# Kernel tuning notes

Measured on AMD Instinct MI355X. Metric: run time of the kernel, lower is better.

Reference implementation:

```python
import jax, jax.numpy as jnp
import numpy as np

B, S, D, M, E, K = 2, 2048, 1024, 1408, 8, 2  # batch, seq, n_embed, n_moe_mlp, n_experts, top_k


def setup_inputs() -> dict:
    key = jax.random.key(0)
    k0, k1, k2, k3, k4 = jax.random.split(key, 5)
    scale = 0.02
    return {
        "x": jax.random.normal(k0, (B, S, D), dtype=jnp.float32),
        "w_gate": jax.random.normal(k1, (D, E), dtype=jnp.float32) * scale,  # gate.weight.T
        "w_g": jax.random.normal(k2, (E, D, M), dtype=jnp.float32) * scale,  # gate_proj.weight.T per expert
        "w_u": jax.random.normal(k3, (E, D, M), dtype=jnp.float32) * scale,  # up_proj.weight.T per expert
        "w_d": jax.random.normal(k4, (E, M, D), dtype=jnp.float32) * scale,  # down_proj.weight.T per expert
    }


def reference(x, w_gate, w_g, w_u, w_d):
    # router
    scores = x @ w_gate                                  # [B,S,E]
    topk_scores, topk_idx = jax.lax.top_k(scores, K)     # [B,S,K]
    topk_probs = jax.nn.softmax(topk_scores, axis=-1)    # softmax over selected experts only
    # scatter top-k probs back to dense [B,S,E] gating (top_k indices are distinct)
    gating = jnp.sum(
        jax.nn.one_hot(topk_idx, E, dtype=topk_probs.dtype) * topk_probs[..., None],
        axis=-2,
    )                                                    # [B,S,E]
    # dense all-expert SwiGLU (faithful to the compute-then-mask original)
    hidden = jax.nn.silu(jnp.einsum("bsd,edm->ebsm", x, w_g)) * jnp.einsum(
        "bsd,edm->ebsm", x, w_u
    )                                                    # [E,B,S,M]
    expert_out = jnp.einsum("ebsm,emd->ebsd", hidden, w_d)  # [E,B,S,D]
    # masked weighted combine
    y = jnp.einsum("bse,ebsd->bsd", gating, expert_out)  # [B,S,D]
    return y
```

## Files before the change

### kernel.cpp

```cpp
#include <hip/hip_runtime.h>
#include <cstdio>

constexpr int T  = 4096;
constexpr int D  = 1024;
constexpr int M  = 1408;
constexpr int E  = 8;

constexpr int TM = 128;
constexpr int TN = 128;
constexpr int BK = 64;
constexpr int RCAP = T * 2 + E * TM;
constexpr int MT_MAX = T / TM;
constexpr int NT_UP = M / TN;
constexpr int NT_DN = D / TN;

constexpr int CSTR = 64;
constexpr int TOKB = 16;
constexpr int RTB  = T / TOKB;
constexpr int TP_PER_W = (M / 32) * (D / 32) * E;
constexpr int PREP_GRID = RTB + 3 * TP_PER_W;

typedef _Float16 half8 __attribute__((ext_vector_type(8)));
typedef _Float16 half4 __attribute__((ext_vector_type(4)));
typedef float    floatx4 __attribute__((ext_vector_type(4)));

constexpr size_t OFF_COUNTS = 0;
constexpr size_t OFF_BASE   = (size_t)E * CSTR * 4;
constexpr size_t OFF_PC     = OFF_BASE + 64;
constexpr size_t OFF_TOTAL  = OFF_PC + 64;
constexpr size_t OFF_T2E    = OFF_TOTAL + 64;
constexpr size_t OFF_T2POS  = OFF_T2E   + (size_t)2 * T * 4;
constexpr size_t OFF_T2P    = OFF_T2POS + (size_t)2 * T * 4;
constexpr size_t OFF_TLIST  = OFF_T2P   + (size_t)2 * T * 4;
constexpr size_t OFF_XG     = OFF_TLIST + (size_t)E * T * 4;
constexpr size_t OFF_HID    = OFF_XG  + (size_t)RCAP * D * 2;
constexpr size_t OFF_WGT    = OFF_HID + (size_t)RCAP * M * 2;
constexpr size_t OFF_WUT    = OFF_WGT + (size_t)E * M * D * 2;
constexpr size_t OFF_WDT    = OFF_WUT + (size_t)E * M * D * 2;
constexpr size_t WS_NEED    = OFF_WDT + (size_t)E * D * M * 2;

__device__ __forceinline__ void gl_lds16(const void* g, void* l) {
  __builtin_amdgcn_global_load_lds(
      (const __attribute__((address_space(1))) unsigned int*)g,
      (__attribute__((address_space(3))) unsigned int*)l, 16, 0, 0);
}

__device__ __forceinline__ void expert_base_pc(const int* __restrict__ counts,
                                               int e, int& base_e, int& pc_e) {
  int b = 0; base_e = 0; pc_e = 0;
  #pragma unroll
  for (int ee = 0; ee < E; ++ee) {
    int c = counts[ee * CSTR];
    int p = (c + TM - 1) / TM * TM;
    if (ee == e) { base_e = b; pc_e = p; }
    b += p;
  }
}

__global__ __launch_bounds__(256) void k_prep(
    const float* __restrict__ x, const float* __restrict__ wgate,
    const float* __restrict__ w_g, const float* __restrict__ w_u,
    const float* __restrict__ w_d,
    _Float16* __restrict__ wgT, _Float16* __restrict__ wuT, _Float16* __restrict__ wdT,
    int* __restrict__ counts, int* __restrict__ tlist,
    int* __restrict__ t2e, int* __restrict__ t2pos, float* __restrict__ t2p) {
  __shared__ float tile[32][33];
  __shared__ int   s_cnt[E];
  __shared__ int   s_base[E];
  __shared__ int   s_e[2 * TOKB];
  __shared__ int   s_pos[2 * TOKB];
  __shared__ float s_p[2 * TOKB];
  int bid = blockIdx.x;

  if (bid < RTB) {
    int wv = threadIdx.x >> 6, lane = threadIdx.x & 63;
    if (threadIdx.x < E) s_cnt[threadIdx.x] = 0;
    __syncthreads();
    for (int j = 0; j < TOKB / 4; ++j) {
      int tl = wv * (TOKB / 4) + j;
      int t  = bid * TOKB + tl;
      const float* xr = x + (size_t)t * D;
      float acc[E] = {0.f,0.f,0.f,0.f,0.f,0.f,0.f,0.f};
      #pragma unroll
      for (int i = 0; i < D / 64; ++i) {
        int d = i * 64 + lane;
        float xv = xr[d];
        const float4* wr2 = (const float4*)(wgate + (size_t)d * E);
        float4 w0 = wr2[0], w1 = wr2[1];
        acc[0] += xv * w0.x; acc[1] += xv * w0.y; acc[2] += xv * w0.z; acc[3] += xv * w0.w;
        acc[4] += xv * w1.x; acc[5] += xv * w1.y; acc[6] += xv * w1.z; acc[7] += xv * w1.w;
      }
      #pragma unroll
      for (int e = 0; e < E; ++e) {
        #pragma unroll
        for (int off = 32; off; off >>= 1) acc[e] += __shfl_xor(acc[e], off, 64);
      }
      if (lane == 0) {
        int i0 = 0; float s0 = acc[0];
        #pragma unroll
        for (int e = 1; e < E; ++e) if (acc[e] > s0) { s0 = acc[e]; i0 = e; }
        int i1 = -1; float s1 = -1e30f;
        #pragma unroll
        for (int e = 0; e < E; ++e) if (e != i0 && acc[e] > s1) { s1 = acc[e]; i1 = e; }
        float p0 = 1.f / (1.f + expf(s1 - s0));
        float p1 = 1.f - p0;
        int q0 = atomicAdd(&s_cnt[i0], 1);
        int q1 = atomicAdd(&s_cnt[i1], 1);
        s_e[2 * tl]     = i0; s_pos[2 * tl]     = q0; s_p[2 * tl]     = p0;
        s_e[2 * tl + 1] = i1; s_pos[2 * tl + 1] = q1; s_p[2 * tl + 1] = p1;
      }
    }
    __syncthreads();
    if (threadIdx.x < E)
      s_base[threadIdx.x] = atomicAdd(&counts[threadIdx.x * CSTR], s_cnt[threadIdx.x]);
    __syncthreads();
    if (threadIdx.x < 2 * TOKB) {
      int sl = threadIdx.x;
      int e = s_e[sl];
      int pos = s_base[e] + s_pos[sl];
      int t = bid * TOKB + (sl >> 1);
      tlist[e * T + pos] = t;
      t2e[2 * t + (sl & 1)]   = e;
      t2pos[2 * t + (sl & 1)] = pos;
      t2p[2 * t + (sl & 1)]   = s_p[sl];
    }
    return;
  }

  int i = bid - RTB;
  int which = i / TP_PER_W;
  int j = i - which * TP_PER_W;
  const float* src; _Float16* dst; int Rr, Cc;
  if (which == 0)      { src = w_g; dst = wgT; Rr = D; Cc = M; }
  else if (which == 1) { src = w_u; dst = wuT; Rr = D; Cc = M; }
  else                 { src = w_d; dst = wdT; Rr = M; Cc = D; }
  int ctn = Cc / 32, rtn = Rr / 32;
  int e   = j / (ctn * rtn);
  int rem = j - e * (ctn * rtn);
  int rt = rem / ctn, ct = rem - rt * ctn;
  int tr  = threadIdx.x >> 3;
  int tc4 = (threadIdx.x & 7) * 4;
  const float* s = src + ((size_t)e * Rr + rt * 32 + tr) * Cc + ct * 32 + tc4;
  float4 v = *(const float4*)s;
  tile[tr][tc4 + 0] = v.x; tile[tr][tc4 + 1] = v.y;
  tile[tr][tc4 + 2] = v.z; tile[tr][tc4 + 3] = v.w;
  __syncthreads();
  union { _Float16 h[4]; ushort4 u; } o;
  #pragma unroll
  for (int q = 0; q < 4; ++q) o.h[q] = (_Float16)tile[tc4 + q][tr];
  *(ushort4*)(dst + ((size_t)e * Cc + ct * 32 + tr) * Rr + rt * 32 + tc4) = o.u;
}

__global__ __launch_bounds__(256) void k_gather(
    const float* __restrict__ x, const int* __restrict__ counts,
    const int* __restrict__ tlist, _Float16* __restrict__ Xg) {
  int r = blockIdx.x;
  int b = 0, e = -1, local = 0, cnt = 0;
  #pragma unroll
  for (int ee = 0; ee < E; ++ee) {
    int c = counts[ee * CSTR];
    int p = (c + TM - 1) / TM * TM;
    if (e < 0 && r < b + p) { e = ee; local = r - b; cnt = c; }
    b += p;
  }
  if (e < 0) return;
  int d = threadIdx.x * 4;
  union { _Float16 h[4]; ushort4 u; } o;
  if (local < cnt) {
    int t = tlist[e * T + local];
    float4 v = *(const float4*)(x + (size_t)t * D + d);
    o.h[0] = (_Float16)v.x; o.h[1] = (_Float16)v.y;
    o.h[2] = (_Float16)v.z; o.h[3] = (_Float16)v.w;
  } else {
    o.h[0] = (_Float16)0.f; o.h[1] = (_Float16)0.f;
    o.h[2] = (_Float16)0.f; o.h[3] = (_Float16)0.f;
  }
  *(ushort4*)(Xg + (size_t)r * D + d) = o.u;
}

__global__ __launch_bounds__(256, 2) void k_upgate(
    const _Float16* __restrict__ Xg, const _Float16* __restrict__ wgT,
    const _Float16* __restrict__ wuT, _Float16* __restrict__ Hid,
    const int* __restrict__ counts) {
  int lin = blockIdx.x;
  int e = lin & 7;
  int r = lin >> 3;
  int nt = r % NT_UP;
  int mt = r / NT_UP;
  int base_e, pc_e;
  expert_base_pc(counts, e, base_e, pc_e);
  if (mt * TM >= pc_e) return;
  int row0 = base_e + mt * TM;
  int n0 = nt * TN;
  __shared__ _Float16 As[TM * BK];
  __shared__ _Float16 Bg[TN * BK];
  __shared__ _Float16 Bu[TN * BK];
  int tid = threadIdx.x;
  int w = tid >> 6, lane = tid & 63;
  int lrow = lane & 15, quad = lane >> 4;
  int wr = w >> 1, wc = w & 1;
  int sr = lane >> 3, sc = (lane & 7) * 8;

  const _Float16* wg_e = wgT + (size_t)e * M * D;
  const _Float16* wu_e = wuT + (size_t)e * M * D;
  const _Float16* pA[4]; const _Float16* pG[4]; const _Float16* pU[4];
  char* lA[4]; char* lG[4]; char* lU[4];
  #pragma unroll
  for (int rr = 0; rr < 4; ++rr) {
    int grow = w * 32 + rr * 8 + sr;
    pA[rr] = Xg   + (size_t)(row0 + grow) * D + sc;
    pG[rr] = wg_e + (size_t)(n0   + grow) * D + sc;
    pU[rr] = wu_e + (size_t)(n0   + grow) * D + sc;
    lA[rr] = (char*)As + (w * 4 + rr) * 1024;
    lG[rr] = (char*)Bg + (w * 4 + rr) * 1024;
    lU[rr] = (char*)Bu + (w * 4 + rr) * 1024;
  }

  floatx4 accg[4][4] = {};
  floatx4 accu[4][4] = {};

  for (int k0 = 0; k0 < D; k0 += BK) {
    #pragma unroll
    for (int rr = 0; rr < 4; ++rr) {
      gl_lds16(pA[rr], lA[rr]);
      gl_lds16(pG[rr], lG[rr]);
      gl_lds16(pU[rr], lU[rr]);
      pA[rr] += BK; pG[rr] += BK; pU[rr] += BK;
    }
    __syncthreads();
    #pragma unroll
    for (int c2 = 0; c2 < 2; ++c2) {
      half8 af[4];
      #pragma unroll
      for (int i = 0; i < 4; ++i)
        af[i] = *(const half8*)&As[(wr * 64 + i * 16 + lrow) * BK + c2 * 32 + quad * 8];
      #pragma unroll
      for (int c = 0; c < 4; ++c) {
        half8 bgc = *(const half8*)&Bg[(wc * 64 + c * 16 + lrow) * BK + c2 * 32 + quad * 8];
        half8 buc = *(const half8*)&Bu[(wc * 64 + c * 16 + lrow) * BK + c2 * 32 + quad * 8];
        #pragma unroll
        for (int i = 0; i < 4; ++i) {
          accg[c][i] = __builtin_amdgcn_mfma_f32_16x16x32_f16(af[i], bgc, accg[c][i], 0, 0, 0);
          accu[c][i] = __builtin_amdgcn_mfma_f32_16x16x32_f16(af[i], buc, accu[c][i], 0, 0, 0);
        }
      }
    }
    __syncthreads();
  }
  #pragma unroll
  for (int c = 0; c < 4; ++c) {
    int col = n0 + wc * 64 + c * 16 + lrow;
    #pragma unroll
    for (int i = 0; i < 4; ++i) {
      int rowb = row0 + wr * 64 + i * 16 + quad * 4;
      #pragma unroll
      for (int reg = 0; reg < 4; ++reg) {
        float g = accg[c][i][reg], u = accu[c][i][reg];
        Hid[(size_t)(rowb + reg) * M + col] = (_Float16)(g / (1.f + expf(-g)) * u);
      }
    }
  }
}

__global__ __launch_bounds__(256, 2) void k_down(
    const _Float16* __restrict__ Hid, const _Float16* __restrict__ wdT,
    _Float16* __restrict__ Yp, const int* __restrict__ counts) {
  int lin = blockIdx.x;
  int e = lin & 7;
  int r = lin >> 3;
  int nt = r % NT_DN;
  int mt = r / NT_DN;
  int base_e, pc_e;
  expert_base_pc(counts, e, base_e, pc_e);
  if (mt * TM >= pc_e) return;
  int row0 = base_e + mt * TM;
  int d0 = nt * TN;
  __shared__ _Float16 As[TM * BK];
  __shared__ _Float16 Bs[TN * BK];
  int tid = threadIdx.x;
  int w = tid >> 6, lane = tid & 63;
  int lrow = lane & 15, quad = lane >> 4;
  int wr = w >> 1, wc = w & 1;
  int sr = lane >> 3, sc = (lane & 7) * 8;

  const _Float16* wd_e = wdT + (size_t)e * D * M;
  const _Float16* pA[4]; const _Float16* pB[4];
  char* lA[4]; char* lB[4];
  #pragma unroll
  for (int rr = 0; rr < 4; ++rr) {
    int grow = w * 32 + rr * 8 + sr;
    pA[rr] = Hid  + (size_t)(row0 + grow) * M + sc;
    pB[rr] = wd_e + (size_t)(d0   + grow) * M + sc;
    lA[rr] = (char*)As + (w * 4 + rr) * 1024;
    lB[rr] = (char*)Bs + (w * 4 + rr) * 1024;
  }

  floatx4 acc[4][4] = {};

  for (int k0 = 0; k0 < M; k0 += BK) {
    #pragma unroll
    for (int rr = 0; rr < 4; ++rr) {
      gl_lds16(pA[rr], lA[rr]);
      gl_lds16(pB[rr], lB[rr]);
      pA[rr] += BK; pB[rr] += BK;
    }
    __syncthreads();
    #pragma unroll
    for (int c2 = 0; c2 < 2; ++c2) {
      half8 af[4];
      #pragma unroll
      for (int i = 0; i < 4; ++i)
        af[i] = *(const half8*)&As[(wr * 64 + i * 16 + lrow) * BK + c2 * 32 + quad * 8];
      #pragma unroll
      for (int c = 0; c < 4; ++c) {
        half8 bc = *(const half8*)&Bs[(wc * 64 + c * 16 + lrow) * BK + c2 * 32 + quad * 8];
        #pragma unroll
        for (int i = 0; i < 4; ++i)
          acc[c][i] = __builtin_amdgcn_mfma_f32_16x16x32_f16(af[i], bc, acc[c][i], 0, 0, 0);
      }
    }
    __syncthreads();
  }
  #pragma unroll
  for (int c = 0; c < 4; ++c) {
    int col = d0 + wc * 64 + c * 16 + lrow;
    #pragma unroll
    for (int i = 0; i < 4; ++i) {
      int rowb = row0 + wr * 64 + i * 16 + quad * 4;
      #pragma unroll
      for (int reg = 0; reg < 4; ++reg)
        Yp[(size_t)(rowb + reg) * D + col] = (_Float16)acc[c][i][reg];
    }
  }
}

__global__ __launch_bounds__(256) void k_combine(
    const _Float16* __restrict__ Yp, const int* __restrict__ counts,
    const int* __restrict__ t2e, const int* __restrict__ t2pos,
    const float* __restrict__ t2p, float* __restrict__ out) {
  int t = blockIdx.x;
  int e0 = t2e[2 * t], e1 = t2e[2 * t + 1];
  int b = 0, b0 = 0, b1 = 0;
  #pragma unroll
  for (int ee = 0; ee < E; ++ee) {
    if (ee == e0) b0 = b;
    if (ee == e1) b1 = b;
    int c = counts[ee * CSTR];
    b += (c + TM - 1) / TM * TM;
  }
  int r0 = b0 + t2pos[2 * t];
  int r1 = b1 + t2pos[2 * t + 1];
  float p0 = t2p[2 * t], p1 = t2p[2 * t + 1];
  int d = threadIdx.x * 4;
  half4 h0 = *(const half4*)(Yp + (size_t)r0 * D + d);
  half4 h1 = *(const half4*)(Yp + (size_t)r1 * D + d);
  float4 o;
  o.x = p0 * (float)h0.x + p1 * (float)h1.x;
  o.y = p0 * (float)h0.y + p1 * (float)h1.y;
  o.z = p0 * (float)h0.z + p1 * (float)h1.z;
  o.w = p0 * (float)h0.w + p1 * (float)h1.w;
  *(float4*)(out + (size_t)t * D + d) = o;
}

extern "C" void kernel_launch(void* const* d_in, const int* in_sizes, int n_in,
                              void* d_out, int out_size, void* d_ws, size_t ws_size,
                              hipStream_t stream) {
  const float* x     = (const float*)d_in[0];
  const float* wgate = (const float*)d_in[1];
  const float* w_g   = (const float*)d_in[2];
  const float* w_u   = (const float*)d_in[3];
  const float* w_d   = (const float*)d_in[4];
  float* out = (float*)d_out;
  char* ws = (char*)d_ws;

  if (ws_size < WS_NEED) {
    fprintf(stderr, "kernel_launch: ws_size=%zu < needed %zu\n", ws_size, WS_NEED);
    return;
  }

  int* counts = (int*)(ws + OFF_COUNTS);
  int* t2e    = (int*)(ws + OFF_T2E);
  int* t2pos  = (int*)(ws + OFF_T2POS);
  float* t2p  = (float*)(ws + OFF_T2P);
  int* tlist  = (int*)(ws + OFF_TLIST);
  _Float16* Xg  = (_Float16*)(ws + OFF_XG);
  _Float16* Hid = (_Float16*)(ws + OFF_HID);
  _Float16* wgT = (_Float16*)(ws + OFF_WGT);
  _Float16* wuT = (_Float16*)(ws + OFF_WUT);
  _Float16* wdT = (_Float16*)(ws + OFF_WDT);

  hipMemsetAsync(counts, 0, (size_t)E * CSTR * 4, stream);

  k_prep<<<PREP_GRID, 256, 0, stream>>>(x, wgate, w_g, w_u, w_d,
                                        wgT, wuT, wdT,
                                        counts, tlist, t2e, t2pos, t2p);
  k_gather<<<RCAP, 256, 0, stream>>>(x, counts, tlist, Xg);
  k_upgate<<<E * MT_MAX * NT_UP, 256, 0, stream>>>(Xg, wgT, wuT, Hid, counts);
  _Float16* Yp = Xg;
  k_down<<<E * MT_MAX * NT_DN, 256, 0, stream>>>(Hid, wdT, Yp, counts);
  k_combine<<<T, 256, 0, stream>>>(Yp, counts, t2e, t2pos, t2p, out);
}
```

Before: 339.1 us.

## Double-buffer LDS in expert GEMMs, swizzle tiles, fold token gather into loads

Both expert GEMM kernels now use two LDS buffers with BK=32, so the next k-slice's global-to-LDS loads are issued while MFMAs run on the current slice. The LDS layout uses an XOR swizzle to reduce bank conflicts on fragment reads. The separate gather kernel is removed: k_prep converts all of x to fp16 and the up/gate kernel indexes token rows through tlist directly. This saves a launch and a padded copy, but the A-tile loads become scattered rows, and the smaller BK doubles the number of barriers.

Result: faster. 308.9 us (-8.9%).

```diff
diff --git a/kernel.cpp b/kernel.cpp
--- a/kernel.cpp
+++ b/kernel.cpp
@@ -8,7 +8,7 @@
 
 constexpr int TM = 128;
 constexpr int TN = 128;
-constexpr int BK = 64;
+constexpr int BK = 32;
 constexpr int RCAP = T * 2 + E * TM;
 constexpr int MT_MAX = T / TM;
 constexpr int NT_UP = M / TN;
@@ -17,8 +17,9 @@
 constexpr int CSTR = 64;
 constexpr int TOKB = 16;
 constexpr int RTB  = T / TOKB;
+constexpr int XCV  = (T * D) / 2048;
 constexpr int TP_PER_W = (M / 32) * (D / 32) * E;
-constexpr int PREP_GRID = RTB + 3 * TP_PER_W;
+constexpr int PREP_GRID = RTB + XCV + 3 * TP_PER_W;
 
 typedef _Float16 half8 __attribute__((ext_vector_type(8)));
 typedef _Float16 half4 __attribute__((ext_vector_type(4)));
@@ -46,13 +47,14 @@
 }
 
 __device__ __forceinline__ void expert_base_pc(const int* __restrict__ counts,
-                                               int e, int& base_e, int& pc_e) {
-  int b = 0; base_e = 0; pc_e = 0;
+                                               int e, int& base_e, int& pc_e,
+                                               int& cnt_e) {
+  int b = 0; base_e = 0; pc_e = 0; cnt_e = 0;
   #pragma unroll
   for (int ee = 0; ee < E; ++ee) {
     int c = counts[ee * CSTR];
     int p = (c + TM - 1) / TM * TM;
-    if (ee == e) { base_e = b; pc_e = p; }
+    if (ee == e) { base_e = b; pc_e = p; cnt_e = c; }
     b += p;
   }
 }
@@ -61,6 +63,7 @@
     const float* __restrict__ x, const float* __restrict__ wgate,
     const float* __restrict__ w_g, const float* __restrict__ w_u,
     const float* __restrict__ w_d,
+    _Float16* __restrict__ Xh,
     _Float16* __restrict__ wgT, _Float16* __restrict__ wuT, _Float16* __restrict__ wdT,
     int* __restrict__ counts, int* __restrict__ tlist,
     int* __restrict__ t2e, int* __restrict__ t2pos, float* __restrict__ t2p) {
@@ -127,7 +130,20 @@
     return;
   }
 
-  int i = bid - RTB;
+  if (bid < RTB + XCV) {
+    size_t base = (size_t)(bid - RTB) * 2048 + threadIdx.x * 8;
+    float4 v0 = *(const float4*)(x + base);
+    float4 v1 = *(const float4*)(x + base + 4);
+    half8 h;
+    h[0] = (_Float16)v0.x; h[1] = (_Float16)v0.y;
+    h[2] = (_Float16)v0.z; h[3] = (_Float16)v0.w;
+    h[4] = (_Float16)v1.x; h[5] = (_Float16)v1.y;
+    h[6] = (_Float16)v1.z; h[7] = (_Float16)v1.w;
+    *(half8*)(Xh + base) = h;
+    return;
+  }
+
+  int i = bid - RTB - XCV;
   int which = i / TP_PER_W;
   int j = i - which * TP_PER_W;
   const float* src; _Float16* dst; int Rr, Cc;
@@ -151,102 +167,92 @@
   *(ushort4*)(dst + ((size_t)e * Cc + ct * 32 + tr) * Rr + rt * 32 + tc4) = o.u;
 }
 
-__global__ __launch_bounds__(256) void k_gather(
-    const float* __restrict__ x, const int* __restrict__ counts,
-    const int* __restrict__ tlist, _Float16* __restrict__ Xg) {
-  int r = blockIdx.x;
-  int b = 0, e = -1, local = 0, cnt = 0;
-  #pragma unroll
-  for (int ee = 0; ee < E; ++ee) {
-    int c = counts[ee * CSTR];
-    int p = (c + TM - 1) / TM * TM;
-    if (e < 0 && r < b + p) { e = ee; local = r - b; cnt = c; }
-    b += p;
-  }
-  if (e < 0) return;
-  int d = threadIdx.x * 4;
-  union { _Float16 h[4]; ushort4 u; } o;
-  if (local < cnt) {
-    int t = tlist[e * T + local];
-    float4 v = *(const float4*)(x + (size_t)t * D + d);
-    o.h[0] = (_Float16)v.x; o.h[1] = (_Float16)v.y;
-    o.h[2] = (_Float16)v.z; o.h[3] = (_Float16)v.w;
-  } else {
-    o.h[0] = (_Float16)0.f; o.h[1] = (_Float16)0.f;
-    o.h[2] = (_Float16)0.f; o.h[3] = (_Float16)0.f;
-  }
-  *(ushort4*)(Xg + (size_t)r * D + d) = o.u;
-}
-
 __global__ __launch_bounds__(256, 2) void k_upgate(
-    const _Float16* __restrict__ Xg, const _Float16* __restrict__ wgT,
+    const _Float16* __restrict__ Xh, const _Float16* __restrict__ wgT,
     const _Float16* __restrict__ wuT, _Float16* __restrict__ Hid,
-    const int* __restrict__ counts) {
+    const int* __restrict__ counts, const int* __restrict__ tlist) {
   int lin = blockIdx.x;
   int e = lin & 7;
   int r = lin >> 3;
   int nt = r % NT_UP;
   int mt = r / NT_UP;
-  int base_e, pc_e;
-  expert_base_pc(counts, e, base_e, pc_e);
+  int base_e, pc_e, cnt_e;
+  expert_base_pc(counts, e, base_e, pc_e, cnt_e);
   if (mt * TM >= pc_e) return;
   int row0 = base_e + mt * TM;
   int n0 = nt * TN;
-  __shared__ _Float16 As[TM * BK];
-  __shared__ _Float16 Bg[TN * BK];
-  __shared__ _Float16 Bu[TN * BK];
+  __shared__ _Float16 As[2][TM * BK];
+  __shared__ _Float16 Bg[2][TN * BK];
+  __shared__ _Float16 Bu[2][TN * BK];
   int tid = threadIdx.x;
   int w = tid >> 6, lane = tid & 63;
   int lrow = lane & 15, quad = lane >> 4;
   int wr = w >> 1, wc = w & 1;
-  int sr = lane >> 3, sc = (lane & 7) * 8;
+  int sr = lane >> 2;
+  int c4 = lane & 3;
+  int swc = ((c4 ^ ((sr >> 1) & 3))) * 8;
 
   const _Float16* wg_e = wgT + (size_t)e * M * D;
   const _Float16* wu_e = wuT + (size_t)e * M * D;
-  const _Float16* pA[4]; const _Float16* pG[4]; const _Float16* pU[4];
-  char* lA[4]; char* lG[4]; char* lU[4];
-  #pragma unroll
-  for (int rr = 0; rr < 4; ++rr) {
-    int grow = w * 32 + rr * 8 + sr;
-    pA[rr] = Xg   + (size_t)(row0 + grow) * D + sc;
-    pG[rr] = wg_e + (size_t)(n0   + grow) * D + sc;
-    pU[rr] = wu_e + (size_t)(n0   + grow) * D + sc;
-    lA[rr] = (char*)As + (w * 4 + rr) * 1024;
-    lG[rr] = (char*)Bg + (w * 4 + rr) * 1024;
-    lU[rr] = (char*)Bu + (w * 4 + rr) * 1024;
-  }
+  const _Float16* pA[2]; const _Float16* pG[2]; const _Float16* pU[2];
+  int loff[2];
+  #pragma unroll
+  for (int is = 0; is < 2; ++is) {
+    int grow = w * 32 + is * 16 + sr;
+    int local = mt * TM + grow;
+    int trow = (local < cnt_e) ? tlist[e * T + local] : 0;
+    pA[is] = Xh   + (size_t)trow * D + swc;
+    pG[is] = wg_e + (size_t)(n0 + grow) * D + swc;
+    pU[is] = wu_e + (size_t)(n0 + grow) * D + swc;
+    loff[is] = (w * 2 + is) * 1024;
+  }
+
+  int swr = (lrow >> 1) & 3;
 
   floatx4 accg[4][4] = {};
   floatx4 accu[4][4] = {};
 
-  for (int k0 = 0; k0 < D; k0 += BK) {
-    #pragma unroll
-    for (int rr = 0; rr < 4; ++rr) {
-      gl_lds16(pA[rr], lA[rr]);
-      gl_lds16(pG[rr], lG[rr]);
-      gl_lds16(pU[rr], lU[rr]);
-      pA[rr] += BK; pG[rr] += BK; pU[rr] += BK;
-    }
+  auto stage = [&](int b) {
+    char* a0 = (char*)&As[b][0];
+    char* g0 = (char*)&Bg[b][0];
+    char* u0 = (char*)&Bu[b][0];
+    #pragma unroll
+    for (int is = 0; is < 2; ++is) {
+      gl_lds16(pA[is], a0 + loff[is]); pA[is] += BK;
+      gl_lds16(pG[is], g0 + loff[is]); pG[is] += BK;
+      gl_lds16(pU[is], u0 + loff[is]); pU[is] += BK;
+    }
+  };
+  auto compute = [&](int b) {
+    int kc = (quad ^ swr) * 8;
+    half8 af[4];
+    #pragma unroll
+    for (int i = 0; i < 4; ++i)
+      af[i] = *(const half8*)&As[b][(wr * 64 + i * 16 + lrow) * BK + kc];
+    #pragma unroll
+    for (int c = 0; c < 4; ++c) {
+      int bo = (wc * 64 + c * 16 + lrow) * BK + kc;
+      half8 bgc = *(const half8*)&Bg[b][bo];
+      half8 buc = *(const half8*)&Bu[b][bo];
+      #pragma unroll
+      for (int i = 0; i < 4; ++i) {
+        accg[c][i] = __builtin_amdgcn_mfma_f32_16x16x32_f16(af[i], bgc, accg[c][i], 0, 0, 0);
+        accu[c][i] = __builtin_amdgcn_mfma_f32_16x16x32_f16(af[i], buc, accu[c][i], 0, 0, 0);
+      }
+    }
+  };
+
+  stage(0);
+  __syncthreads();
+  int cur = 0;
+  for (int kt = 1; kt < D / BK; ++kt) {
+    stage(cur ^ 1);
+    compute(cur);
     __syncthreads();
-    #pragma unroll
-    for (int c2 = 0; c2 < 2; ++c2) {
-      half8 af[4];
-      #pragma unroll
-      for (int i = 0; i < 4; ++i)
-        af[i] = *(const half8*)&As[(wr * 64 + i * 16 + lrow) * BK + c2 * 32 + quad * 8];
-      #pragma unroll
-      for (int c = 0; c < 4; ++c) {
-        half8 bgc = *(const half8*)&Bg[(wc * 64 + c * 16 + lrow) * BK + c2 * 32 + quad * 8];
-        half8 buc = *(const half8*)&Bu[(wc * 64 + c * 16 + lrow) * BK + c2 * 32 + quad * 8];
-        #pragma unroll
-        for (int i = 0; i < 4; ++i) {
-          accg[c][i] = __builtin_amdgcn_mfma_f32_16x16x32_f16(af[i], bgc, accg[c][i], 0, 0, 0);
-          accu[c][i] = __builtin_amdgcn_mfma_f32_16x16x32_f16(af[i], buc, accu[c][i], 0, 0, 0);
-        }
-      }
-    }
-    __syncthreads();
-  }
+    cur ^= 1;
+  }
+  compute(cur);
+
   #pragma unroll
   for (int c = 0; c < 4; ++c) {
     int col = n0 + wc * 64 + c * 16 + lrow;
@@ -270,57 +276,71 @@
   int r = lin >> 3;
   int nt = r % NT_DN;
   int mt = r / NT_DN;
-  int base_e, pc_e;
-  expert_base_pc(counts, e, base_e, pc_e);
+  int base_e, pc_e, cnt_e;
+  expert_base_pc(counts, e, base_e, pc_e, cnt_e);
   if (mt * TM >= pc_e) return;
   int row0 = base_e + mt * TM;
   int d0 = nt * TN;
-  __shared__ _Float16 As[TM * BK];
-  __shared__ _Float16 Bs[TN * BK];
+  __shared__ _Float16 As[2][TM * BK];
+  __shared__ _Float16 Bs[2][TN * BK];
   int tid = threadIdx.x;
   int w = tid >> 6, lane = tid & 63;
   int lrow = lane & 15, quad = lane >> 4;
   int wr = w >> 1, wc = w & 1;
-  int sr = lane >> 3, sc = (lane & 7) * 8;
+  int sr = lane >> 2;
+  int c4 = lane & 3;
+  int swc = ((c4 ^ ((sr >> 1) & 3))) * 8;
 
   const _Float16* wd_e = wdT + (size_t)e * D * M;
-  const _Float16* pA[4]; const _Float16* pB[4];
-  char* lA[4]; char* lB[4];
-  #pragma unroll
-  for (int rr = 0; rr < 4; ++rr) {
-    int grow = w * 32 + rr * 8 + sr;
-    pA[rr] = Hid  + (size_t)(row0 + grow) * M + sc;
-    pB[rr] = wd_e + (size_t)(d0   + grow) * M + sc;
-    lA[rr] = (char*)As + (w * 4 + rr) * 1024;
-    lB[rr] = (char*)Bs + (w * 4 + rr) * 1024;
-  }
+  const _Float16* pA[2]; const _Float16* pB[2];
+  int loff[2];
+  #pragma unroll
+  for (int is = 0; is < 2; ++is) {
+    int grow = w * 32 + is * 16 + sr;
+    pA[is] = Hid  + (size_t)(row0 + grow) * M + swc;
+    pB[is] = wd_e + (size_t)(d0   + grow) * M + swc;
+    loff[is] = (w * 2 + is) * 1024;
+  }
+
+  int swr = (lrow >> 1) & 3;
 
   floatx4 acc[4][4] = {};
 
-  for (int k0 = 0; k0 < M; k0 += BK) {
-    #pragma unroll
-    for (int rr = 0; rr < 4; ++rr) {
-      gl_lds16(pA[rr], lA[rr]);
-      gl_lds16(pB[rr], lB[rr]);
-      pA[rr] += BK; pB[rr] += BK;
-    }
+  auto stage = [&](int b) {
+    char* a0 = (char*)&As[b][0];
+    char* b0 = (char*)&Bs[b][0];
+    #pragma unroll
+    for (int is = 0; is < 2; ++is) {
+      gl_lds16(pA[is], a0 + loff[is]); pA[is] += BK;
+      gl_lds16(pB[is], b0 + loff[is]); pB[is] += BK;
+    }
+  };
+  auto compute = [&](int b) {
+    int kc = (quad ^ swr) * 8;
+    half8 af[4];
+    #pragma unroll
+    for (int i = 0; i < 4; ++i)
+      af[i] = *(const half8*)&As[b][(wr * 64 + i * 16 + lrow) * BK + kc];
+    #pragma unroll
+    for (int c = 0; c < 4; ++c) {
+      half8 bc = *(const half8*)&Bs[b][(wc * 64 + c * 16 + lrow) * BK + kc];
+      #pragma unroll
+      for (int i = 0; i < 4; ++i)
+        acc[c][i] = __builtin_amdgcn_mfma_f32_16x16x32_f16(af[i], bc, acc[c][i], 0, 0, 0);
+    }
+  };
+
+  stage(0);
+  __syncthreads();
+  int cur = 0;
+  for (int kt = 1; kt < M / BK; ++kt) {
+    stage(cur ^ 1);
+    compute(cur);
     __syncthreads();
-    #pragma unroll
-    for (int c2 = 0; c2 < 2; ++c2) {
-      half8 af[4];
-      #pragma unroll
-      for (int i = 0; i < 4; ++i)
-        af[i] = *(const half8*)&As[(wr * 64 + i * 16 + lrow) * BK + c2 * 32 + quad * 8];
-      #pragma unroll
-      for (int c = 0; c < 4; ++c) {
-        half8 bc = *(const half8*)&Bs[(wc * 64 + c * 16 + lrow) * BK + c2 * 32 + quad * 8];
-        #pragma unroll
-        for (int i = 0; i < 4; ++i)
-          acc[c][i] = __builtin_amdgcn_mfma_f32_16x16x32_f16(af[i], bc, acc[c][i], 0, 0, 0);
-      }
-    }
-    __syncthreads();
-  }
+    cur ^= 1;
+  }
+  compute(cur);
+
   #pragma unroll
   for (int c = 0; c < 4; ++c) {
     int col = d0 + wc * 64 + c * 16 + lrow;
@@ -383,7 +403,7 @@
   int* t2pos  = (int*)(ws + OFF_T2POS);
   float* t2p  = (float*)(ws + OFF_T2P);
   int* tlist  = (int*)(ws + OFF_TLIST);
-  _Float16* Xg  = (_Float16*)(ws + OFF_XG);
+  _Float16* Xh  = (_Float16*)(ws + OFF_XG);
   _Float16* Hid = (_Float16*)(ws + OFF_HID);
   _Float16* wgT = (_Float16*)(ws + OFF_WGT);
   _Float16* wuT = (_Float16*)(ws + OFF_WUT);
@@ -391,12 +411,11 @@
 
   hipMemsetAsync(counts, 0, (size_t)E * CSTR * 4, stream);
 
-  k_prep<<<PREP_GRID, 256, 0, stream>>>(x, wgate, w_g, w_u, w_d,
+  k_prep<<<PREP_GRID, 256, 0, stream>>>(x, wgate, w_g, w_u, w_d, Xh,
                                         wgT, wuT, wdT,
                                         counts, tlist, t2e, t2pos, t2p);
-  k_gather<<<RCAP, 256, 0, stream>>>(x, counts, tlist, Xg);
-  k_upgate<<<E * MT_MAX * NT_UP, 256, 0, stream>>>(Xg, wgT, wuT, Hid, counts);
-  _Float16* Yp = Xg;
+  k_upgate<<<E * MT_MAX * NT_UP, 256, 0, stream>>>(Xh, wgT, wuT, Hid, counts, tlist);
+  _Float16* Yp = Xh;
   k_down<<<E * MT_MAX * NT_DN, 256, 0, stream>>>(Hid, wdT, Yp, counts);
   k_combine<<<T, 256, 0, stream>>>(Yp, counts, t2e, t2pos, t2p, out);
 }
```
